# Optimization experiments

Measured on AMD Instinct MI355X. Metric: run time of the kernel, lower is better.

Reference implementation:

```python
import jax, jax.numpy as jnp
import numpy as np

NPOINT, NSAMPLE, RADIUS = 2048, 32, 0.2
EPS = 1e-5


def setup_inputs() -> dict:
    key = jax.random.key(0)
    ks = jax.random.split(key, 12)
    B, N, C = 8, 8192, 64
    mlp = [64, 64, 128]
    inp = {
        "xyz": jax.random.normal(ks[0], (B, 3, N), dtype=jnp.float32),
        "points": jax.random.normal(ks[1], (B, C, N), dtype=jnp.float32),
    }
    last = C + 3  # use_xyz concatenates 3 relative coords
    for i, out in enumerate(mlp, 1):
        inp[f"W{i}"] = jax.random.normal(ks[2 * i], (out, last), dtype=jnp.float32) / np.sqrt(last).astype(np.float32)
        inp[f"b{i}"] = jnp.zeros((out,), jnp.float32)
        inp[f"g{i}"] = jnp.ones((out,), jnp.float32)
        inp[f"be{i}"] = jnp.zeros((out,), jnp.float32)
        last = out
    return inp


def fps(xyz_t, npoint):
    """Farthest point sampling. xyz_t: (B,N,3) -> (B,npoint) int32 indices."""
    xyz_t = jax.lax.stop_gradient(xyz_t)  # indices are non-differentiable
    B, N, _ = xyz_t.shape

    def step(carry, _):
        dists, far = carry  # (B,N), (B,)
        cent = jnp.take_along_axis(xyz_t, far[:, None, None], axis=1)  # (B,1,3)
        d = jnp.sum((xyz_t - cent) ** 2, axis=-1)
        dists = jnp.minimum(dists, d)
        nf = jnp.argmax(dists, axis=-1).astype(jnp.int32)
        return (dists, nf), far

    init = (jnp.full((B, N), 1e10, xyz_t.dtype), jnp.zeros((B,), jnp.int32))
    _, idxs = jax.lax.scan(step, init, None, length=npoint)
    return jnp.transpose(idxs)  # (B, npoint)


def ball_query(xyz_t, new_xyz_t, radius, nsample):
    """First-nsample-in-radius neighbor indices, padded with first hit.
    xyz_t (B,N,3), new_xyz_t (B,M,3) -> (B,M,nsample) int32."""
    B, N, _ = xyz_t.shape
    # squared distances via gemm to avoid (B,M,N,3) intermediate
    sq = (jnp.sum(new_xyz_t ** 2, -1)[:, :, None]
          + jnp.sum(xyz_t ** 2, -1)[:, None, :]
          - 2.0 * jnp.einsum('bmd,bnd->bmn', new_xyz_t, xyz_t))  # (B,M,N)
    cand = jnp.where(sq < radius * radius, jnp.arange(N, dtype=jnp.int32), N)
    idx = jnp.sort(cand, axis=-1)[:, :, :nsample]  # first k in-radius by index order
    first = idx[:, :, :1]
    first = jnp.where(first == N, 0, first)  # guard empty groups
    idx = jnp.where(idx == N, first, idx)
    return idx


def group(feat, idx):
    """feat (B,C,N), idx (B,M,k) -> (B,C,M,k) gathered neighbor features."""
    return jnp.take_along_axis(feat[:, :, None, :], idx[:, None, :, :], axis=3)


def conv_bn_relu(x, W, b, g, be):
    """Shared 1x1 Conv2d + BatchNorm2d (batch stats, training mode) + ReLU.
    x: (B,C,M,K) -> (B,O,M,K)."""
    y = jnp.einsum('oc,bcmk->bomk', W, x) + b[None, :, None, None]
    mu = jnp.mean(y, axis=(0, 2, 3), keepdims=True)
    var = jnp.var(y, axis=(0, 2, 3), keepdims=True)
    y = (y - mu) * jax.lax.rsqrt(var + EPS)
    y = y * g[None, :, None, None] + be[None, :, None, None]
    return jax.nn.relu(y)


def reference(xyz, points, W1, b1, g1, be1, W2, b2, g2, be2, W3, b3, g3, be3):
    xyz_t = jnp.transpose(xyz, (0, 2, 1))  # (B,N,3)
    fidx = fps(xyz_t, NPOINT)  # (B,M)
    new_xyz = jnp.take_along_axis(xyz, fidx[:, None, :], axis=2)  # (B,3,M)
    idx = ball_query(xyz_t, jnp.transpose(new_xyz, (0, 2, 1)), RADIUS, NSAMPLE)  # (B,M,K)
    grouped_xyz = group(xyz, idx) - new_xyz[:, :, :, None]  # (B,3,M,K) centered
    grouped_pts = group(points, idx)  # (B,f,M,K)
    x = jnp.concatenate([grouped_xyz, grouped_pts], axis=1)  # (B,f+3,M,K)
    x = conv_bn_relu(x, W1, b1, g1, be1)
    x = conv_bn_relu(x, W2, b2, g2, be2)
    x = conv_bn_relu(x, W3, b3, g3, be3)
    new_points = jnp.max(x, axis=3)  # (B,mlp[-1],M)
    return (new_xyz, new_points)
```

## Files before the change

### kernel.cpp

```cpp
#include <hip/hip_runtime.h>

#define BB 8
#define NN 8192
#define MM 2048
#define KK 32
#define NTOT (BB*MM*KK)

#define WS_PTS_T  0
#define WS_XYZN   4194304
#define WS_IDX    5242880
#define WS_GPART  5767168
#define WS_PARAMS 6291456
#define WS_ZMAX   6292480
#define WS_ZMIN   8389632
#define WS_TOTAL  10486784

typedef float v2f __attribute__((ext_vector_type(2)));

__global__ __launch_bounds__(256) void k_transpose(const float* __restrict__ pts,
                                                   float* __restrict__ pts_t){
  __shared__ float tile[64][65];
  int bid = blockIdx.x;
  int b = bid >> 7;
  int n0 = (bid & 127) << 6;
  int tx = threadIdx.x & 63, ty = threadIdx.x >> 6;
  const float* src = pts + (size_t)b*64*NN;
  #pragma unroll
  for (int c = ty; c < 64; c += 4)
    tile[c][tx] = src[(size_t)c*NN + n0 + tx];
  __syncthreads();
  float* dst = pts_t + ((size_t)b*NN + n0)*64;
  #pragma unroll
  for (int r = ty; r < 64; r += 4)
    dst[(size_t)r*64 + tx] = tile[tx][r];
}

__global__ __launch_bounds__(256) void k_xyzn(const float* __restrict__ xyz,
                                              float4* __restrict__ xyzn){
  #pragma clang fp contract(off)
  int i = blockIdx.x*256 + threadIdx.x;
  int b = i >> 13, n = i & 8191;
  const float* p = xyz + (size_t)b*3*NN;
  float x = p[n], y = p[NN+n], z = p[2*NN+n];
  float nrm = (x*x + y*y) + z*z;
  xyzn[i] = make_float4(x, y, z, nrm);
}

#define DPPMAXF(ctrl, rmask)                                                 \
  {                                                                          \
    float s_ = __int_as_float(__builtin_amdgcn_update_dpp(                   \
        __float_as_int(m), __float_as_int(m), (ctrl), (rmask), 0xf, false)); \
    m = fmaxf(m, s_);                                                        \
  }

__global__ __launch_bounds__(256,1) void k_fps(const float* __restrict__ xyz,
                                               float* __restrict__ out_newxyz){
  #pragma clang fp contract(off)
  __shared__ float4 sp4[NN];
  __shared__ unsigned long long swk[2][4];
  int b = blockIdx.x, tid = threadIdx.x;
  const float* xb = xyz + (size_t)b*3*NN;
  int n0 = tid << 5;
  v2f px[16], py[16], pz[16], dd[16];
  const float4* xb4 = (const float4*)xb;
  #pragma unroll
  for (int q = 0; q < 8; ++q){
    float4 X = xb4[(n0>>2) + q];
    float4 Y = xb4[(NN>>2) + (n0>>2) + q];
    float4 Z = xb4[((2*NN)>>2) + (n0>>2) + q];
    px[2*q]   = (v2f){X.x, X.y}; px[2*q+1] = (v2f){X.z, X.w};
    py[2*q]   = (v2f){Y.x, Y.y}; py[2*q+1] = (v2f){Y.z, Y.w};
    pz[2*q]   = (v2f){Z.x, Z.y}; pz[2*q+1] = (v2f){Z.z, Z.w};
    dd[2*q]   = (v2f){1e10f,1e10f}; dd[2*q+1] = (v2f){1e10f,1e10f};
    sp4[n0+4*q+0] = make_float4(X.x, Y.x, Z.x, 0.f);
    sp4[n0+4*q+1] = make_float4(X.y, Y.y, Z.y, 0.f);
    sp4[n0+4*q+2] = make_float4(X.z, Y.z, Z.z, 0.f);
    sp4[n0+4*q+3] = make_float4(X.w, Y.w, Z.w, 0.f);
  }
  __syncthreads();
  float4 c0 = sp4[0];
  float cx = c0.x, cy = c0.y, cz = c0.z;
  float* ob = out_newxyz + (size_t)b*3*MM;
  int lane = tid & 63, wid = tid >> 6;
  for (int s = 0; s < 8; ++s){
    float ox = 0.f, oy = 0.f, oz = 0.f;
    #pragma unroll 1
    for (int ti = 0; ti < 256; ++ti){
      if (tid == ti){ ox = cx; oy = cy; oz = cz; }
      v2f cvx = (v2f){cx,cx}, cvy = (v2f){cy,cy}, cvz = (v2f){cz,cz};
      v2f bv2 = (v2f){-1.f,-1.f};
      #pragma unroll
      for (int g = 0; g < 16; ++g){
        v2f dx = px[g]-cvx, dy = py[g]-cvy, dz = pz[g]-cvz;
        v2f xx = dx*dx, yy = dy*dy, zz = dz*dz;
        v2f sm = xx + yy;
        v2f d  = sm + zz;
        v2f nd = __builtin_elementwise_min(dd[g], d);
        dd[g] = nd;
        bv2 = __builtin_elementwise_max(bv2, nd);
      }
      float bv = fmaxf(bv2.x, bv2.y);
      float m = bv;
      DPPMAXF(0x111, 0xf)
      DPPMAXF(0x112, 0xf)
      DPPMAXF(0x114, 0xf)
      DPPMAXF(0x118, 0xf)
      DPPMAXF(0x142, 0xa)
      DPPMAXF(0x143, 0xc)
      float wm = __int_as_float(__builtin_amdgcn_readlane(__float_as_int(m), 63));
      unsigned long long msk = __ballot(bv == wm);
      int wl = (int)__builtin_ctzll(msk);
      int bj = 0;
      #pragma unroll
      for (int g = 15; g >= 0; --g){
        if (dd[g].y == bv) bj = 2*g+1;
        if (dd[g].x == bv) bj = 2*g;
      }
      int nwin = __builtin_amdgcn_readlane(n0 + bj, wl);
      int buf = ti & 1;
      if (lane == 0){
        unsigned long long key =
            ((unsigned long long)__float_as_uint(wm) << 32) |
            (unsigned int)(~(unsigned int)nwin);
        swk[buf][wid] = key;
      }
      __syncthreads();
      const unsigned long long* kk = swk[buf];
      unsigned long long k0=kk[0], k1=kk[1], k2=kk[2], k3=kk[3];
      unsigned long long a = (k0>k1)?k0:k1, c2 = (k2>k3)?k2:k3;
      unsigned long long kmax = (a>c2)?a:c2;
      int far = (int)(~(unsigned int)kmax) & (NN-1);
      float4 c4 = sp4[far];
      cx = c4.x; cy = c4.y; cz = c4.z;
    }
    ob[(s<<8)+tid] = ox; ob[MM+(s<<8)+tid] = oy; ob[2*MM+(s<<8)+tid] = oz;
  }
}

__global__ __launch_bounds__(256) void k_ballq(const float4* __restrict__ xyzn,
                                               const float* __restrict__ newxyz,
                                               int* __restrict__ idx){
  #pragma clang fp contract(off)
  __shared__ unsigned long long s_mask[32][129];
  __shared__ float4 s_c4[32];
  const float R2 = (float)(0.2*0.2);
  int b = blockIdx.x >> 6;
  int m0 = (blockIdx.x & 63) << 5;
  int tid = threadIdx.x, lane = tid & 63, wv = tid >> 6;
  const float* nb = newxyz + (size_t)b*3*MM;
  if (tid < 32){
    int m = m0 + tid;
    float cx = nb[m], cy = nb[MM+m], cz = nb[2*MM+m];
    float cn = (cx*cx + cy*cy) + cz*cz;
    s_c4[tid] = make_float4(cx, cy, cz, cn);
  }
  __syncthreads();
  const float4* src = xyzn + (size_t)b*NN;
  for (int ci = 0; ci < 32; ++ci){
    int ch = ci*4 + wv;
    float4 p = src[ch*64 + lane];
    #pragma unroll 8
    for (int mi = 0; mi < 32; ++mi){
      float4 c = s_c4[mi];
      float dot = (c.x*p.x + c.y*p.y) + c.z*p.z;
      float sq = (c.w + p.w) - 2.0f*dot;
      unsigned long long mk = __ballot(sq < R2);
      if (lane == 0) s_mask[mi][ch] = mk;
    }
  }
  __syncthreads();
  if (tid < 32){
    int m = m0 + tid;
    int* om = idx + ((size_t)(b*MM + m))*KK;
    int filled = 0, first = -1;
    for (int ch = 0; ch < 128 && filled < KK; ++ch){
      unsigned long long mk = s_mask[tid][ch];
      while (mk){
        int bp = __builtin_ctzll(mk);
        mk &= mk - 1;
        int j = ch*64 + bp;
        if (first < 0) first = j;
        om[filled++] = j;
        if (filled == KK) break;
      }
    }
    int pad = (first < 0) ? 0 : first;
    for (int s = filled; s < KK; ++s) om[s] = pad;
  }
}

#define XST 260
#define PST 66

__device__ __forceinline__ void fma_po(float4& a0, float4& a1, float w,
                                       const float4& xA, const float4& xB){
  a0.x = fmaf(w, xA.x, a0.x); a0.y = fmaf(w, xA.y, a0.y);
  a0.z = fmaf(w, xA.z, a0.z); a0.w = fmaf(w, xA.w, a0.w);
  a1.x = fmaf(w, xB.x, a1.x); a1.y = fmaf(w, xB.y, a1.y);
  a1.z = fmaf(w, xB.z, a1.z); a1.w = fmaf(w, xB.w, a1.w);
}

__device__ __forceinline__ void gemm_step(float4 (&acc)[8][2], const float* sw,
                                          const float* sx, int c, int ob8, int pb){
  float4 xA = *(const float4*)&sx[c*XST + pb];
  float4 xB = *(const float4*)&sx[c*XST + pb + 4];
  float4 wA = *(const float4*)&sw[c*64 + ob8];
  float4 wB = *(const float4*)&sw[c*64 + ob8 + 4];
  fma_po(acc[0][0], acc[0][1], wA.x, xA, xB);
  fma_po(acc[1][0], acc[1][1], wA.y, xA, xB);
  fma_po(acc[2][0], acc[2][1], wA.z, xA, xB);
  fma_po(acc[3][0], acc[3][1], wA.w, xA, xB);
  fma_po(acc[4][0], acc[4][1], wB.x, xA, xB);
  fma_po(acc[5][0], acc[5][1], wB.y, xA, xB);
  fma_po(acc[6][0], acc[6][1], wB.z, xA, xB);
  fma_po(acc[7][0], acc[7][1], wB.w, xA, xB);
}

__device__ __forceinline__ void gather_col(float* sx, const float* pts_t,
    const float4* xyzn, const float* nb, const int* idx, int b, int bid, int tid){
  int m0 = (bid & 255) << 3;
  int m = m0 + (tid >> 5), k = tid & 31;
  int j = idx[((size_t)(b*MM + m))*KK + k];
  float4 P = xyzn[(size_t)b*NN + j];
  sx[0*XST + tid] = P.x - nb[m];
  sx[1*XST + tid] = P.y - nb[MM+m];
  sx[2*XST + tid] = P.z - nb[2*MM+m];
  const float4* pf = (const float4*)(pts_t + ((size_t)b*NN + j)*64);
  #pragma unroll
  for (int c4 = 0; c4 < 16; ++c4){
    float4 v = pf[c4];
    sx[(3+4*c4+0)*XST + tid] = v.x;
    sx[(3+4*c4+1)*XST + tid] = v.y;
    sx[(3+4*c4+2)*XST + tid] = v.z;
    sx[(3+4*c4+3)*XST + tid] = v.w;
  }
}

__device__ __forceinline__ void tile_stats(const float4 (&acc)[8][2], float* s_pp,
    float* gpart, int ob8, int pg, int tid, int bid, int nch_base){
  #pragma unroll
  for (int oi = 0; oi < 8; ++oi){
    float4 a0 = acc[oi][0], a1 = acc[oi][1];
    float s  = ((a0.x+a0.y)+(a0.z+a0.w)) + ((a1.x+a1.y)+(a1.z+a1.w));
    float q2 = ((a0.x*a0.x + a0.y*a0.y) + (a0.z*a0.z + a0.w*a0.w))
             + ((a1.x*a1.x + a1.y*a1.y) + (a1.z*a1.z + a1.w*a1.w));
    int o = ob8 + oi;
    s_pp[o*PST + pg*2 + 0] = s;
    s_pp[o*PST + pg*2 + 1] = q2;
  }
  __syncthreads();
  if (tid < 128){
    int o = tid >> 1, st = tid & 1;
    float S = 0.f;
    #pragma unroll 8
    for (int q = 0; q < 32; ++q) S += s_pp[o*PST + q*2 + st];
    gpart[(size_t)(st*128 + nch_base + o)*2048 + bid] = S;
  }
}

__global__ __launch_bounds__(256,1) void k_conv1_stats(const float* __restrict__ pts_t,
    const float4* __restrict__ xyzn, const float* __restrict__ newxyz,
    const int* __restrict__ idx, const float* __restrict__ W1, float* __restrict__ gpart){
  __shared__ float s_w1[67*64];
  __shared__ float s_x[67*XST];
  int tid = threadIdx.x;
  for (int i = tid; i < 67*64; i += 256){ int c = i>>6, o = i&63; s_w1[i] = W1[o*67 + c]; }
  int bid = blockIdx.x, b = bid >> 8;
  const float* nb = newxyz + (size_t)b*3*MM;
  gather_col(s_x, pts_t, xyzn, nb, idx, b, bid, tid);
  __syncthreads();
  int oq = tid & 7, pg = tid >> 3;
  int ob8 = oq*8, pb = pg*8;
  float4 acc[8][2];
  #pragma unroll
  for (int oi=0;oi<8;++oi){ acc[oi][0]=make_float4(0,0,0,0); acc[oi][1]=make_float4(0,0,0,0); }
  for (int c = 0; c < 67; ++c) gemm_step(acc, s_w1, s_x, c, ob8, pb);
  __syncthreads();
  tile_stats(acc, s_x, gpart, ob8, pg, tid, bid, 0);
}

__global__ __launch_bounds__(256,1) void k_conv2_stats(const float* __restrict__ pts_t,
    const float4* __restrict__ xyzn, const float* __restrict__ newxyz,
    const int* __restrict__ idx, const float* __restrict__ W1, const float* __restrict__ W2,
    const float* __restrict__ params1, float* __restrict__ gpart){
  __shared__ float s_w1[67*64];
  __shared__ float s_w2[64*64];
  __shared__ float s_p[128];
  __shared__ float s_x[67*XST];
  int tid = threadIdx.x;
  for (int i = tid; i < 67*64; i += 256){ int c = i>>6, o = i&63; s_w1[i] = W1[o*67 + c]; }
  for (int i = tid; i < 64*64; i += 256){ int c = i>>6, o = i&63; s_w2[i] = W2[o*64 + c]; }
  if (tid < 64){ s_p[tid] = params1[tid]; s_p[64+tid] = params1[128+tid]; }
  int bid = blockIdx.x, b = bid >> 8;
  const float* nb = newxyz + (size_t)b*3*MM;
  gather_col(s_x, pts_t, xyzn, nb, idx, b, bid, tid);
  __syncthreads();
  int oq = tid & 7, pg = tid >> 3;
  int ob8 = oq*8, pb = pg*8;
  float4 acc[8][2];
  #pragma unroll
  for (int oi=0;oi<8;++oi){ acc[oi][0]=make_float4(0,0,0,0); acc[oi][1]=make_float4(0,0,0,0); }
  for (int c = 0; c < 67; ++c) gemm_step(acc, s_w1, s_x, c, ob8, pb);
  float4 hreg[8][2];
  #pragma unroll
  for (int oi = 0; oi < 8; ++oi){
    float A = s_p[ob8+oi], C = s_p[64+ob8+oi];
    float4 z0 = acc[oi][0], z1 = acc[oi][1], h0, h1;
    h0.x = fmaxf(fmaf(A, z0.x, C), 0.f); h0.y = fmaxf(fmaf(A, z0.y, C), 0.f);
    h0.z = fmaxf(fmaf(A, z0.z, C), 0.f); h0.w = fmaxf(fmaf(A, z0.w, C), 0.f);
    h1.x = fmaxf(fmaf(A, z1.x, C), 0.f); h1.y = fmaxf(fmaf(A, z1.y, C), 0.f);
    h1.z = fmaxf(fmaf(A, z1.z, C), 0.f); h1.w = fmaxf(fmaf(A, z1.w, C), 0.f);
    hreg[oi][0] = h0; hreg[oi][1] = h1;
  }
  __syncthreads();
  #pragma unroll
  for (int oi = 0; oi < 8; ++oi){
    *(float4*)&s_x[(ob8+oi)*XST + pb]     = hreg[oi][0];
    *(float4*)&s_x[(ob8+oi)*XST + pb + 4] = hreg[oi][1];
  }
  __syncthreads();
  #pragma unroll
  for (int oi=0;oi<8;++oi){ acc[oi][0]=make_float4(0,0,0,0); acc[oi][1]=make_float4(0,0,0,0); }
  for (int c = 0; c < 64; ++c) gemm_step(acc, s_w2, s_x, c, ob8, pb);
  __syncthreads();
  tile_stats(acc, s_x, gpart, ob8, pg, tid, bid, 0);
}

__device__ __forceinline__ void accum_ch(float4* acc, const float4* w4, int c, float v){
  #pragma unroll
  for (int o4 = 0; o4 < 16; ++o4){
    float4 w = w4[c*16 + o4];
    acc[o4].x = fmaf(w.x, v, acc[o4].x);
    acc[o4].y = fmaf(w.y, v, acc[o4].y);
    acc[o4].z = fmaf(w.z, v, acc[o4].z);
    acc[o4].w = fmaf(w.w, v, acc[o4].w);
  }
}

__device__ __forceinline__ void conv1_pos(float4* acc, const float* s_w1,
    const float* pts_t, const float4* xyzn, const float* nb, int b, int m, int j){
  #pragma unroll
  for (int o4 = 0; o4 < 16; ++o4) acc[o4] = make_float4(0.f,0.f,0.f,0.f);
  float4 P = xyzn[(size_t)b*NN + j];
  float x0 = P.x - nb[m], x1 = P.y - nb[MM+m], x2 = P.z - nb[2*MM+m];
  const float4* w4 = (const float4*)s_w1;
  accum_ch(acc, w4, 0, x0);
  accum_ch(acc, w4, 1, x1);
  accum_ch(acc, w4, 2, x2);
  const float4* pf = (const float4*)(pts_t + ((size_t)b*NN + j)*64);
  #pragma unroll
  for (int c4 = 0; c4 < 16; ++c4){
    float4 v = pf[c4];
    accum_ch(acc, w4, 3+4*c4+0, v.x);
    accum_ch(acc, w4, 3+4*c4+1, v.y);
    accum_ch(acc, w4, 3+4*c4+2, v.z);
    accum_ch(acc, w4, 3+4*c4+3, v.w);
  }
}

__global__ __launch_bounds__(256) void k_bnfin(const float* __restrict__ gpart,
    const float* __restrict__ g, const float* __restrict__ be, float* __restrict__ params){
  int o = blockIdx.x, t = threadIdx.x;
  double s = 0.0, sq = 0.0;
  for (int i = t; i < 2048; i += 256){
    s  += (double)gpart[(size_t)o*2048 + i];
    sq += (double)gpart[(size_t)(128+o)*2048 + i];
  }
  __shared__ double ds[256], dq[256];
  ds[t] = s; dq[t] = sq; __syncthreads();
  for (int off = 128; off > 0; off >>= 1){
    if (t < off){ ds[t] += ds[t+off]; dq[t] += dq[t+off]; }
    __syncthreads();
  }
  if (t == 0){
    double mu = ds[0] / (double)NTOT;
    double var = dq[0] / (double)NTOT - mu*mu;
    float A = g[o] / sqrtf((float)var + 1e-5f);
    float Cc = be[o] - (float)mu * A;
    params[o] = A; params[128+o] = Cc;
  }
}

__global__ __launch_bounds__(256,1) void k_conv3(const float* __restrict__ pts_t,
    const float4* __restrict__ xyzn, const float* __restrict__ newxyz,
    const int* __restrict__ idx, const float* __restrict__ W1, const float* __restrict__ W2,
    const float* __restrict__ W3, const float* __restrict__ params1,
    const float* __restrict__ params2, float* __restrict__ gpart,
    float* __restrict__ zmax, float* __restrict__ zmin){
  __shared__ float s_w1[67*64];
  __shared__ float s_w2[64*64];
  __shared__ float s_p[256];
  __shared__ float s_z[256*68];
  __shared__ float s_sm[8*128*2];
  int tid = threadIdx.x;
  for (int i = tid; i < 67*64; i += 256){ int c = i>>6, o = i&63; s_w1[i] = W1[o*67 + c]; }
  for (int i = tid; i < 64*64; i += 256){ int c = i>>6, o = i&63; s_w2[i] = W2[o*64 + c]; }
  if (tid < 64){
    s_p[tid]      = params1[tid];     s_p[64+tid]  = params1[128+tid];
    s_p[128+tid]  = params2[tid];     s_p[192+tid] = params2[128+tid];
  }
  __syncthreads();
  int bid = blockIdx.x, b = bid >> 8, m0 = (bid & 255) << 3;
  {
    int m = m0 + (tid >> 5), k = tid & 31;
    int j = idx[((size_t)(b*MM + m))*KK + k];
    const float* nb = newxyz + (size_t)b*3*MM;
    float4 acc[16];
    conv1_pos(acc, s_w1, pts_t, xyzn, nb, b, m, j);
    float4 h[16];
    #pragma unroll
    for (int o4 = 0; o4 < 16; ++o4){
      float4 z = acc[o4], hh;
      hh.x = fmaxf(fmaf(s_p[4*o4+0], z.x, s_p[64+4*o4+0]), 0.f);
      hh.y = fmaxf(fmaf(s_p[4*o4+1], z.y, s_p[64+4*o4+1]), 0.f);
      hh.z = fmaxf(fmaf(s_p[4*o4+2], z.z, s_p[64+4*o4+2]), 0.f);
      hh.w = fmaxf(fmaf(s_p[4*o4+3], z.w, s_p[64+4*o4+3]), 0.f);
      h[o4] = hh;
    }
    float4 a2[16];
    #pragma unroll
    for (int o4 = 0; o4 < 16; ++o4) a2[o4] = make_float4(0.f,0.f,0.f,0.f);
    const float4* w24 = (const float4*)s_w2;
    #pragma unroll
    for (int c4 = 0; c4 < 16; ++c4){
      accum_ch(a2, w24, 4*c4+0, h[c4].x);
      accum_ch(a2, w24, 4*c4+1, h[c4].y);
      accum_ch(a2, w24, 4*c4+2, h[c4].z);
      accum_ch(a2, w24, 4*c4+3, h[c4].w);
    }
    #pragma unroll
    for (int o4 = 0; o4 < 16; ++o4){
      float4 z = a2[o4], hh;
      hh.x = fmaxf(fmaf(s_p[128+4*o4+0], z.x, s_p[192+4*o4+0]), 0.f);
      hh.y = fmaxf(fmaf(s_p[128+4*o4+1], z.y, s_p[192+4*o4+1]), 0.f);
      hh.z = fmaxf(fmaf(s_p[128+4*o4+2], z.z, s_p[192+4*o4+2]), 0.f);
      hh.w = fmaxf(fmaf(s_p[128+4*o4+3], z.w, s_p[192+4*o4+3]), 0.f);
      *(float4*)&s_z[tid*68 + o4*4] = hh;
    }
  }
  __syncthreads();
  int ml = tid >> 5, og = tid & 31;
  float accK[4][32];
  #pragma unroll
  for (int oo = 0; oo < 4; ++oo)
    #pragma unroll
    for (int k2 = 0; k2 < 32; ++k2) accK[oo][k2] = 0.f;
  const float4* w3g = (const float4*)W3;
  #pragma unroll
  for (int c4 = 0; c4 < 16; ++c4){
    float4 w[4];
    #pragma unroll
    for (int oo = 0; oo < 4; ++oo) w[oo] = w3g[(og*4+oo)*16 + c4];
    #pragma unroll
    for (int k2 = 0; k2 < 32; ++k2){
      float4 hv = *(const float4*)&s_z[(ml*32+k2)*68 + c4*4];
      #pragma unroll
      for (int oo = 0; oo < 4; ++oo){
        accK[oo][k2] = fmaf(w[oo].x, hv.x, accK[oo][k2]);
        accK[oo][k2] = fmaf(w[oo].y, hv.y, accK[oo][k2]);
        accK[oo][k2] = fmaf(w[oo].z, hv.z, accK[oo][k2]);
        accK[oo][k2] = fmaf(w[oo].w, hv.w, accK[oo][k2]);
      }
    }
  }
  int m = m0 + ml;
  #pragma unroll
  for (int oo = 0; oo < 4; ++oo){
    float mx = -3.4e38f, mn = 3.4e38f, s = 0.f, sq = 0.f;
    #pragma unroll
    for (int k2 = 0; k2 < 32; ++k2){
      float v = accK[oo][k2];
      mx = fmaxf(mx, v); mn = fminf(mn, v);
      s += v; sq = fmaf(v, v, sq);
    }
    int o = og*4 + oo;
    zmax[((size_t)(b*128 + o))*MM + m] = mx;
    zmin[((size_t)(b*128 + o))*MM + m] = mn;
    s_sm[(ml*128+o)*2] = s; s_sm[(ml*128+o)*2+1] = sq;
  }
  __syncthreads();
  {
    int o = tid >> 1, st = tid & 1;
    float S = 0.f;
    #pragma unroll
    for (int mm = 0; mm < 8; ++mm) S += s_sm[(mm*128+o)*2 + st];
    gpart[(size_t)(st*128+o)*2048 + bid] = S;
  }
}

__global__ __launch_bounds__(256) void k_out(const float* __restrict__ zmax,
    const float* __restrict__ zmin, const float* __restrict__ params3,
    float* __restrict__ out){
  int i = blockIdx.x*256 + threadIdx.x;
  int o = (i >> 11) & 127;
  float A = params3[o], Cc = params3[128+o];
  float v = (A >= 0.f) ? fmaf(A, zmax[i], Cc) : fmaf(A, zmin[i], Cc);
  out[49152 + i] = fmaxf(v, 0.f);
}

extern "C" void kernel_launch(void* const* d_in, const int* in_sizes, int n_in,
                              void* d_out, int out_size, void* d_ws, size_t ws_size,
                              hipStream_t stream){
  const float* xyz    = (const float*)d_in[0];
  const float* points = (const float*)d_in[1];
  const float* W1  = (const float*)d_in[2];
  const float* g1  = (const float*)d_in[4];
  const float* be1 = (const float*)d_in[5];
  const float* W2  = (const float*)d_in[6];
  const float* g2  = (const float*)d_in[8];
  const float* be2 = (const float*)d_in[9];
  const float* W3  = (const float*)d_in[10];
  const float* g3  = (const float*)d_in[12];
  const float* be3 = (const float*)d_in[13];

  if (ws_size < (size_t)WS_TOTAL * sizeof(float)) return;

  float*  ws     = (float*)d_ws;
  float*  pts_t  = ws + WS_PTS_T;
  float4* xyzn   = (float4*)(ws + WS_XYZN);
  int*    idx    = (int*)(ws + WS_IDX);
  float*  gpart  = ws + WS_GPART;
  float*  params = ws + WS_PARAMS;
  float*  zmax   = ws + WS_ZMAX;
  float*  zmin   = ws + WS_ZMIN;
  float*  out    = (float*)d_out;
  float*  newxyz = out;

  hipLaunchKernelGGL(k_fps,       dim3(8),    dim3(256), 0, stream, xyz, newxyz);
  hipLaunchKernelGGL(k_transpose, dim3(1024), dim3(256), 0, stream, points, pts_t);
  hipLaunchKernelGGL(k_xyzn,      dim3(256),  dim3(256), 0, stream, xyz, xyzn);
  hipLaunchKernelGGL(k_ballq,     dim3(512),  dim3(256), 0, stream, xyzn, newxyz, idx);
  hipLaunchKernelGGL(k_conv1_stats, dim3(2048), dim3(256), 0, stream,
                     pts_t, xyzn, newxyz, idx, W1, gpart);
  hipLaunchKernelGGL(k_bnfin, dim3(64), dim3(256), 0, stream, gpart, g1, be1, params+0);
  hipLaunchKernelGGL(k_conv2_stats, dim3(2048), dim3(256), 0, stream,
                     pts_t, xyzn, newxyz, idx, W1, W2, params+0, gpart);
  hipLaunchKernelGGL(k_bnfin, dim3(64), dim3(256), 0, stream, gpart, g2, be2, params+256);
  hipLaunchKernelGGL(k_conv3, dim3(2048), dim3(256), 0, stream,
                     pts_t, xyzn, newxyz, idx, W1, W2, W3, params+0, params+256,
                     gpart, zmax, zmin);
  hipLaunchKernelGGL(k_bnfin, dim3(128), dim3(256), 0, stream, gpart, g3, be3, params+512);
  hipLaunchKernelGGL(k_out, dim3(8192), dim3(256), 0, stream, zmax, zmin, params+512, out);
}
```

Baseline: 2.792 ms.

## Process two batches per FPS block with 512 threads; tile conv3 GEMMs via shared memory

FPS now runs 4 blocks of 512 threads, each handling two batch items with interleaved updates and reductions. Each thread holds 16 points instead of 32, and centroid coordinates are read from the global xyzn buffer instead of an LDS copy, so k_xyzn now launches before FPS. This targets FPS's serial per-iteration latency by overlapping two independent dependency chains, at the cost of more registers and 8-wave reductions. Separately, conv3 replaces its per-thread 67→64→64 recompute with the shared-memory tiled gather/GEMM path used by conv2, and stages W3 in LDS, which raises LDS use per block.

```diff
diff --git a/kernel.cpp b/kernel.cpp
--- a/kernel.cpp
+++ b/kernel.cpp
@@ -46,94 +46,120 @@
   xyzn[i] = make_float4(x, y, z, nrm);
 }
 
-#define DPPMAXF(ctrl, rmask)                                                 \
-  {                                                                          \
-    float s_ = __int_as_float(__builtin_amdgcn_update_dpp(                   \
-        __float_as_int(m), __float_as_int(m), (ctrl), (rmask), 0xf, false)); \
-    m = fmaxf(m, s_);                                                        \
-  }
-
-__global__ __launch_bounds__(256,1) void k_fps(const float* __restrict__ xyz,
+__device__ __forceinline__ float wave_max_f32(float v){
+#define WMSTEP(c,r) { float s_ = __int_as_float(__builtin_amdgcn_update_dpp(   \
+      __float_as_int(v), __float_as_int(v), (c), (r), 0xf, false));            \
+    v = fmaxf(v, s_); }
+  WMSTEP(0x111, 0xf)
+  WMSTEP(0x112, 0xf)
+  WMSTEP(0x114, 0xf)
+  WMSTEP(0x118, 0xf)
+  WMSTEP(0x142, 0xa)
+  WMSTEP(0x143, 0xc)
+#undef WMSTEP
+  return __int_as_float(__builtin_amdgcn_readlane(__float_as_int(v), 63));
+}
+
+__device__ __forceinline__ float fps_update(v2f* px, v2f* py, v2f* pz, v2f* dd,
+                                            float cx, float cy, float cz){
+  v2f cvx = (v2f){cx,cx}, cvy = (v2f){cy,cy}, cvz = (v2f){cz,cz};
+  v2f bv2 = (v2f){-1.f,-1.f};
+  #pragma unroll
+  for (int g = 0; g < 8; ++g){
+    v2f dx = px[g]-cvx, dy = py[g]-cvy, dz = pz[g]-cvz;
+    v2f xx = dx*dx, yy = dy*dy, zz = dz*dz;
+    v2f sm = xx + yy;
+    v2f d  = sm + zz;
+    v2f nd = __builtin_elementwise_min(dd[g], d);
+    dd[g] = nd;
+    bv2 = __builtin_elementwise_max(bv2, nd);
+  }
+  return fmaxf(bv2.x, bv2.y);
+}
+
+__device__ __forceinline__ void fps_reduce(float bv, const v2f* dd, int n0,
+    int lane, int wid, unsigned long long* swk){
+  float wm = wave_max_f32(bv);
+  unsigned long long msk = __ballot(bv == wm);
+  int wl = (int)__builtin_ctzll(msk);
+  int bj = 0;
+  #pragma unroll
+  for (int g = 7; g >= 0; --g){
+    if (dd[g].y == bv) bj = 2*g+1;
+    if (dd[g].x == bv) bj = 2*g;
+  }
+  int nw = __builtin_amdgcn_readlane(n0 + bj, wl);
+  if (lane == 0)
+    swk[wid] = ((unsigned long long)__float_as_uint(wm) << 32) |
+               (unsigned int)(~(unsigned int)nw);
+}
+
+__device__ __forceinline__ unsigned long long tree8(const unsigned long long* k){
+  unsigned long long a = (k[0]>k[1])?k[0]:k[1], b = (k[2]>k[3])?k[2]:k[3];
+  unsigned long long c = (k[4]>k[5])?k[4]:k[5], d = (k[6]>k[7])?k[6]:k[7];
+  unsigned long long e = (a>b)?a:b, f = (c>d)?c:d;
+  return (e>f)?e:f;
+}
+
+__global__ __launch_bounds__(512,1) void k_fps(const float* __restrict__ xyz,
+                                               const float4* __restrict__ xyzn,
                                                float* __restrict__ out_newxyz){
   #pragma clang fp contract(off)
-  __shared__ float4 sp4[NN];
-  __shared__ unsigned long long swk[2][4];
-  int b = blockIdx.x, tid = threadIdx.x;
-  const float* xb = xyz + (size_t)b*3*NN;
-  int n0 = tid << 5;
-  v2f px[16], py[16], pz[16], dd[16];
+  __shared__ unsigned long long swk[2][2][8];
+  int tid = threadIdx.x, lane = tid & 63, wid = tid >> 6;
+  int bA = blockIdx.x*2, bB = bA + 1;
+  const float* xa = xyz + (size_t)bA*3*NN;
+  const float* xb = xyz + (size_t)bB*3*NN;
+  int n0 = tid << 4;
+  v2f pxA[8],pyA[8],pzA[8],ddA[8];
+  v2f pxB[8],pyB[8],pzB[8],ddB[8];
+  const float4* xa4 = (const float4*)xa;
   const float4* xb4 = (const float4*)xb;
   #pragma unroll
-  for (int q = 0; q < 8; ++q){
-    float4 X = xb4[(n0>>2) + q];
-    float4 Y = xb4[(NN>>2) + (n0>>2) + q];
-    float4 Z = xb4[((2*NN)>>2) + (n0>>2) + q];
-    px[2*q]   = (v2f){X.x, X.y}; px[2*q+1] = (v2f){X.z, X.w};
-    py[2*q]   = (v2f){Y.x, Y.y}; py[2*q+1] = (v2f){Y.z, Y.w};
-    pz[2*q]   = (v2f){Z.x, Z.y}; pz[2*q+1] = (v2f){Z.z, Z.w};
-    dd[2*q]   = (v2f){1e10f,1e10f}; dd[2*q+1] = (v2f){1e10f,1e10f};
-    sp4[n0+4*q+0] = make_float4(X.x, Y.x, Z.x, 0.f);
-    sp4[n0+4*q+1] = make_float4(X.y, Y.y, Z.y, 0.f);
-    sp4[n0+4*q+2] = make_float4(X.z, Y.z, Z.z, 0.f);
-    sp4[n0+4*q+3] = make_float4(X.w, Y.w, Z.w, 0.f);
-  }
-  __syncthreads();
-  float4 c0 = sp4[0];
-  float cx = c0.x, cy = c0.y, cz = c0.z;
-  float* ob = out_newxyz + (size_t)b*3*MM;
-  int lane = tid & 63, wid = tid >> 6;
-  for (int s = 0; s < 8; ++s){
-    float ox = 0.f, oy = 0.f, oz = 0.f;
+  for (int q = 0; q < 4; ++q){
+    float4 X = xa4[(n0>>2)+q];
+    float4 Y = xa4[(NN>>2)+(n0>>2)+q];
+    float4 Z = xa4[((2*NN)>>2)+(n0>>2)+q];
+    pxA[2*q] = (v2f){X.x,X.y}; pxA[2*q+1] = (v2f){X.z,X.w};
+    pyA[2*q] = (v2f){Y.x,Y.y}; pyA[2*q+1] = (v2f){Y.z,Y.w};
+    pzA[2*q] = (v2f){Z.x,Z.y}; pzA[2*q+1] = (v2f){Z.z,Z.w};
+    ddA[2*q] = (v2f){1e10f,1e10f}; ddA[2*q+1] = (v2f){1e10f,1e10f};
+    X = xb4[(n0>>2)+q];
+    Y = xb4[(NN>>2)+(n0>>2)+q];
+    Z = xb4[((2*NN)>>2)+(n0>>2)+q];
+    pxB[2*q] = (v2f){X.x,X.y}; pxB[2*q+1] = (v2f){X.z,X.w};
+    pyB[2*q] = (v2f){Y.x,Y.y}; pyB[2*q+1] = (v2f){Y.z,Y.w};
+    pzB[2*q] = (v2f){Z.x,Z.y}; pzB[2*q+1] = (v2f){Z.z,Z.w};
+    ddB[2*q] = (v2f){1e10f,1e10f}; ddB[2*q+1] = (v2f){1e10f,1e10f};
+  }
+  float4 c0A = xyzn[(size_t)bA*NN];
+  float4 c0B = xyzn[(size_t)bB*NN];
+  float cxA=c0A.x, cyA=c0A.y, czA=c0A.z;
+  float cxB=c0B.x, cyB=c0B.y, czB=c0B.z;
+  float* obA = out_newxyz + (size_t)bA*3*MM;
+  float* obB = out_newxyz + (size_t)bB*3*MM;
+  for (int s = 0; s < 4; ++s){
+    float oxA=0,oyA=0,ozA=0, oxB=0,oyB=0,ozB=0;
     #pragma unroll 1
-    for (int ti = 0; ti < 256; ++ti){
-      if (tid == ti){ ox = cx; oy = cy; oz = cz; }
-      v2f cvx = (v2f){cx,cx}, cvy = (v2f){cy,cy}, cvz = (v2f){cz,cz};
-      v2f bv2 = (v2f){-1.f,-1.f};
-      #pragma unroll
-      for (int g = 0; g < 16; ++g){
-        v2f dx = px[g]-cvx, dy = py[g]-cvy, dz = pz[g]-cvz;
-        v2f xx = dx*dx, yy = dy*dy, zz = dz*dz;
-        v2f sm = xx + yy;
-        v2f d  = sm + zz;
-        v2f nd = __builtin_elementwise_min(dd[g], d);
-        dd[g] = nd;
-        bv2 = __builtin_elementwise_max(bv2, nd);
-      }
-      float bv = fmaxf(bv2.x, bv2.y);
-      float m = bv;
-      DPPMAXF(0x111, 0xf)
-      DPPMAXF(0x112, 0xf)
-      DPPMAXF(0x114, 0xf)
-      DPPMAXF(0x118, 0xf)
-      DPPMAXF(0x142, 0xa)
-      DPPMAXF(0x143, 0xc)
-      float wm = __int_as_float(__builtin_amdgcn_readlane(__float_as_int(m), 63));
-      unsigned long long msk = __ballot(bv == wm);
-      int wl = (int)__builtin_ctzll(msk);
-      int bj = 0;
-      #pragma unroll
-      for (int g = 15; g >= 0; --g){
-        if (dd[g].y == bv) bj = 2*g+1;
-        if (dd[g].x == bv) bj = 2*g;
-      }
-      int nwin = __builtin_amdgcn_readlane(n0 + bj, wl);
+    for (int ti = 0; ti < 512; ++ti){
+      if (tid == ti){ oxA=cxA; oyA=cyA; ozA=czA; oxB=cxB; oyB=cyB; ozB=czB; }
+      float bvA = fps_update(pxA,pyA,pzA,ddA, cxA,cyA,czA);
+      float bvB = fps_update(pxB,pyB,pzB,ddB, cxB,cyB,czB);
       int buf = ti & 1;
-      if (lane == 0){
-        unsigned long long key =
-            ((unsigned long long)__float_as_uint(wm) << 32) |
-            (unsigned int)(~(unsigned int)nwin);
-        swk[buf][wid] = key;
-      }
+      fps_reduce(bvA, ddA, n0, lane, wid, swk[buf][0]);
+      fps_reduce(bvB, ddB, n0, lane, wid, swk[buf][1]);
       __syncthreads();
-      const unsigned long long* kk = swk[buf];
-      unsigned long long k0=kk[0], k1=kk[1], k2=kk[2], k3=kk[3];
-      unsigned long long a = (k0>k1)?k0:k1, c2 = (k2>k3)?k2:k3;
-      unsigned long long kmax = (a>c2)?a:c2;
-      int far = (int)(~(unsigned int)kmax) & (NN-1);
-      float4 c4 = sp4[far];
-      cx = c4.x; cy = c4.y; cz = c4.z;
+      unsigned long long kmA = tree8(swk[buf][0]);
+      unsigned long long kmB = tree8(swk[buf][1]);
+      int farA = (int)(~(unsigned int)kmA) & (NN-1);
+      int farB = (int)(~(unsigned int)kmB) & (NN-1);
+      float4 c4A = xyzn[(size_t)bA*NN + farA];
+      float4 c4B = xyzn[(size_t)bB*NN + farB];
+      cxA=c4A.x; cyA=c4A.y; czA=c4A.z;
+      cxB=c4B.x; cyB=c4B.y; czB=c4B.z;
     }
-    ob[(s<<8)+tid] = ox; ob[MM+(s<<8)+tid] = oy; ob[2*MM+(s<<8)+tid] = oz;
+    obA[(s<<9)+tid] = oxA; obA[MM+(s<<9)+tid] = oyA; obA[2*MM+(s<<9)+tid] = ozA;
+    obB[(s<<9)+tid] = oxB; obB[MM+(s<<9)+tid] = oyB; obB[2*MM+(s<<9)+tid] = ozB;
   }
 }
 
@@ -236,6 +262,29 @@
   }
 }
 
+__device__ __forceinline__ void bnrelu_tile(float4 (&acc)[8][2], const float* sA,
+                                            const float* sC, int ob8){
+  #pragma unroll
+  for (int oi = 0; oi < 8; ++oi){
+    float A = sA[ob8+oi], C = sC[ob8+oi];
+    float4 z0 = acc[oi][0], z1 = acc[oi][1];
+    z0.x = fmaxf(fmaf(A, z0.x, C), 0.f); z0.y = fmaxf(fmaf(A, z0.y, C), 0.f);
+    z0.z = fmaxf(fmaf(A, z0.z, C), 0.f); z0.w = fmaxf(fmaf(A, z0.w, C), 0.f);
+    z1.x = fmaxf(fmaf(A, z1.x, C), 0.f); z1.y = fmaxf(fmaf(A, z1.y, C), 0.f);
+    z1.z = fmaxf(fmaf(A, z1.z, C), 0.f); z1.w = fmaxf(fmaf(A, z1.w, C), 0.f);
+    acc[oi][0] = z0; acc[oi][1] = z1;
+  }
+}
+
+__device__ __forceinline__ void stash_tile(const float4 (&acc)[8][2], float* sx,
+                                           int ob8, int pb){
+  #pragma unroll
+  for (int oi = 0; oi < 8; ++oi){
+    *(float4*)&sx[(ob8+oi)*XST + pb]     = acc[oi][0];
+    *(float4*)&sx[(ob8+oi)*XST + pb + 4] = acc[oi][1];
+  }
+}
+
 __device__ __forceinline__ void tile_stats(const float4 (&acc)[8][2], float* s_pp,
     float* gpart, int ob8, int pg, int tid, int bid, int nch_base){
   #pragma unroll
@@ -301,61 +350,15 @@
   #pragma unroll
   for (int oi=0;oi<8;++oi){ acc[oi][0]=make_float4(0,0,0,0); acc[oi][1]=make_float4(0,0,0,0); }
   for (int c = 0; c < 67; ++c) gemm_step(acc, s_w1, s_x, c, ob8, pb);
-  float4 hreg[8][2];
-  #pragma unroll
-  for (int oi = 0; oi < 8; ++oi){
-    float A = s_p[ob8+oi], C = s_p[64+ob8+oi];
-    float4 z0 = acc[oi][0], z1 = acc[oi][1], h0, h1;
-    h0.x = fmaxf(fmaf(A, z0.x, C), 0.f); h0.y = fmaxf(fmaf(A, z0.y, C), 0.f);
-    h0.z = fmaxf(fmaf(A, z0.z, C), 0.f); h0.w = fmaxf(fmaf(A, z0.w, C), 0.f);
-    h1.x = fmaxf(fmaf(A, z1.x, C), 0.f); h1.y = fmaxf(fmaf(A, z1.y, C), 0.f);
-    h1.z = fmaxf(fmaf(A, z1.z, C), 0.f); h1.w = fmaxf(fmaf(A, z1.w, C), 0.f);
-    hreg[oi][0] = h0; hreg[oi][1] = h1;
-  }
-  __syncthreads();
-  #pragma unroll
-  for (int oi = 0; oi < 8; ++oi){
-    *(float4*)&s_x[(ob8+oi)*XST + pb]     = hreg[oi][0];
-    *(float4*)&s_x[(ob8+oi)*XST + pb + 4] = hreg[oi][1];
-  }
+  bnrelu_tile(acc, s_p, s_p+64, ob8);
+  __syncthreads();
+  stash_tile(acc, s_x, ob8, pb);
   __syncthreads();
   #pragma unroll
   for (int oi=0;oi<8;++oi){ acc[oi][0]=make_float4(0,0,0,0); acc[oi][1]=make_float4(0,0,0,0); }
   for (int c = 0; c < 64; ++c) gemm_step(acc, s_w2, s_x, c, ob8, pb);
   __syncthreads();
   tile_stats(acc, s_x, gpart, ob8, pg, tid, bid, 0);
-}
-
-__device__ __forceinline__ void accum_ch(float4* acc, const float4* w4, int c, float v){
-  #pragma unroll
-  for (int o4 = 0; o4 < 16; ++o4){
-    float4 w = w4[c*16 + o4];
-    acc[o4].x = fmaf(w.x, v, acc[o4].x);
-    acc[o4].y = fmaf(w.y, v, acc[o4].y);
-    acc[o4].z = fmaf(w.z, v, acc[o4].z);
-    acc[o4].w = fmaf(w.w, v, acc[o4].w);
-  }
-}
-
-__device__ __forceinline__ void conv1_pos(float4* acc, const float* s_w1,
-    const float* pts_t, const float4* xyzn, const float* nb, int b, int m, int j){
-  #pragma unroll
-  for (int o4 = 0; o4 < 16; ++o4) acc[o4] = make_float4(0.f,0.f,0.f,0.f);
-  float4 P = xyzn[(size_t)b*NN + j];
-  float x0 = P.x - nb[m], x1 = P.y - nb[MM+m], x2 = P.z - nb[2*MM+m];
-  const float4* w4 = (const float4*)s_w1;
-  accum_ch(acc, w4, 0, x0);
-  accum_ch(acc, w4, 1, x1);
-  accum_ch(acc, w4, 2, x2);
-  const float4* pf = (const float4*)(pts_t + ((size_t)b*NN + j)*64);
-  #pragma unroll
-  for (int c4 = 0; c4 < 16; ++c4){
-    float4 v = pf[c4];
-    accum_ch(acc, w4, 3+4*c4+0, v.x);
-    accum_ch(acc, w4, 3+4*c4+1, v.y);
-    accum_ch(acc, w4, 3+4*c4+2, v.z);
-    accum_ch(acc, w4, 3+4*c4+3, v.w);
-  }
 }
 
 __global__ __launch_bounds__(256) void k_bnfin(const float* __restrict__ gpart,
@@ -389,55 +392,38 @@
     float* __restrict__ zmax, float* __restrict__ zmin){
   __shared__ float s_w1[67*64];
   __shared__ float s_w2[64*64];
+  __shared__ float s_w3[64*128];
   __shared__ float s_p[256];
-  __shared__ float s_z[256*68];
+  __shared__ float s_x[67*XST];
   __shared__ float s_sm[8*128*2];
   int tid = threadIdx.x;
   for (int i = tid; i < 67*64; i += 256){ int c = i>>6, o = i&63; s_w1[i] = W1[o*67 + c]; }
   for (int i = tid; i < 64*64; i += 256){ int c = i>>6, o = i&63; s_w2[i] = W2[o*64 + c]; }
+  for (int i = tid; i < 64*128; i += 256){ int c = i>>7, o = i&127; s_w3[c*128+o] = W3[o*64 + c]; }
   if (tid < 64){
     s_p[tid]      = params1[tid];     s_p[64+tid]  = params1[128+tid];
     s_p[128+tid]  = params2[tid];     s_p[192+tid] = params2[128+tid];
   }
-  __syncthreads();
   int bid = blockIdx.x, b = bid >> 8, m0 = (bid & 255) << 3;
-  {
-    int m = m0 + (tid >> 5), k = tid & 31;
-    int j = idx[((size_t)(b*MM + m))*KK + k];
-    const float* nb = newxyz + (size_t)b*3*MM;
-    float4 acc[16];
-    conv1_pos(acc, s_w1, pts_t, xyzn, nb, b, m, j);
-    float4 h[16];
-    #pragma unroll
-    for (int o4 = 0; o4 < 16; ++o4){
-      float4 z = acc[o4], hh;
-      hh.x = fmaxf(fmaf(s_p[4*o4+0], z.x, s_p[64+4*o4+0]), 0.f);
-      hh.y = fmaxf(fmaf(s_p[4*o4+1], z.y, s_p[64+4*o4+1]), 0.f);
-      hh.z = fmaxf(fmaf(s_p[4*o4+2], z.z, s_p[64+4*o4+2]), 0.f);
-      hh.w = fmaxf(fmaf(s_p[4*o4+3], z.w, s_p[64+4*o4+3]), 0.f);
-      h[o4] = hh;
-    }
-    float4 a2[16];
-    #pragma unroll
-    for (int o4 = 0; o4 < 16; ++o4) a2[o4] = make_float4(0.f,0.f,0.f,0.f);
-    const float4* w24 = (const float4*)s_w2;
-    #pragma unroll
-    for (int c4 = 0; c4 < 16; ++c4){
-      accum_ch(a2, w24, 4*c4+0, h[c4].x);
-      accum_ch(a2, w24, 4*c4+1, h[c4].y);
-      accum_ch(a2, w24, 4*c4+2, h[c4].z);
-      accum_ch(a2, w24, 4*c4+3, h[c4].w);
-    }
-    #pragma unroll
-    for (int o4 = 0; o4 < 16; ++o4){
-      float4 z = a2[o4], hh;
-      hh.x = fmaxf(fmaf(s_p[128+4*o4+0], z.x, s_p[192+4*o4+0]), 0.f);
-      hh.y = fmaxf(fmaf(s_p[128+4*o4+1], z.y, s_p[192+4*o4+1]), 0.f);
-      hh.z = fmaxf(fmaf(s_p[128+4*o4+2], z.z, s_p[192+4*o4+2]), 0.f);
-      hh.w = fmaxf(fmaf(s_p[128+4*o4+3], z.w, s_p[192+4*o4+3]), 0.f);
-      *(float4*)&s_z[tid*68 + o4*4] = hh;
-    }
-  }
+  const float* nb = newxyz + (size_t)b*3*MM;
+  gather_col(s_x, pts_t, xyzn, nb, idx, b, bid, tid);
+  __syncthreads();
+  int oq = tid & 7, pg = tid >> 3;
+  int ob8 = oq*8, pb = pg*8;
+  float4 acc[8][2];
+  #pragma unroll
+  for (int oi=0;oi<8;++oi){ acc[oi][0]=make_float4(0,0,0,0); acc[oi][1]=make_float4(0,0,0,0); }
+  for (int c = 0; c < 67; ++c) gemm_step(acc, s_w1, s_x, c, ob8, pb);
+  bnrelu_tile(acc, s_p, s_p+64, ob8);
+  __syncthreads();
+  stash_tile(acc, s_x, ob8, pb);
+  __syncthreads();
+  #pragma unroll
+  for (int oi=0;oi<8;++oi){ acc[oi][0]=make_float4(0,0,0,0); acc[oi][1]=make_float4(0,0,0,0); }
+  for (int c = 0; c < 64; ++c) gemm_step(acc, s_w2, s_x, c, ob8, pb);
+  bnrelu_tile(acc, s_p+128, s_p+192, ob8);
+  __syncthreads();
+  stash_tile(acc, s_x, ob8, pb);
   __syncthreads();
   int ml = tid >> 5, og = tid & 31;
   float accK[4][32];
@@ -445,21 +431,19 @@
   for (int oo = 0; oo < 4; ++oo)
     #pragma unroll
     for (int k2 = 0; k2 < 32; ++k2) accK[oo][k2] = 0.f;
-  const float4* w3g = (const float4*)W3;
-  #pragma unroll
-  for (int c4 = 0; c4 < 16; ++c4){
-    float4 w[4];
+  for (int c = 0; c < 64; ++c){
+    float4 w = *(const float4*)&s_w3[c*128 + og*4];
     #pragma unroll
-    for (int oo = 0; oo < 4; ++oo) w[oo] = w3g[(og*4+oo)*16 + c4];
-    #pragma unroll
-    for (int k2 = 0; k2 < 32; ++k2){
-      float4 hv = *(const float4*)&s_z[(ml*32+k2)*68 + c4*4];
+    for (int q = 0; q < 8; ++q){
+      float4 xv = *(const float4*)&s_x[c*XST + ml*32 + q*4];
+      float xs4[4] = {xv.x, xv.y, xv.z, xv.w};
       #pragma unroll
-      for (int oo = 0; oo < 4; ++oo){
-        accK[oo][k2] = fmaf(w[oo].x, hv.x, accK[oo][k2]);
-        accK[oo][k2] = fmaf(w[oo].y, hv.y, accK[oo][k2]);
-        accK[oo][k2] = fmaf(w[oo].z, hv.z, accK[oo][k2]);
-        accK[oo][k2] = fmaf(w[oo].w, hv.w, accK[oo][k2]);
+      for (int j = 0; j < 4; ++j){
+        float xs = xs4[j];
+        accK[0][q*4+j] = fmaf(w.x, xs, accK[0][q*4+j]);
+        accK[1][q*4+j] = fmaf(w.y, xs, accK[1][q*4+j]);
+        accK[2][q*4+j] = fmaf(w.z, xs, accK[2][q*4+j]);
+        accK[3][q*4+j] = fmaf(w.w, xs, accK[3][q*4+j]);
       }
     }
   }
@@ -526,9 +510,9 @@
   float*  out    = (float*)d_out;
   float*  newxyz = out;
 
-  hipLaunchKernelGGL(k_fps,       dim3(8),    dim3(256), 0, stream, xyz, newxyz);
+  hipLaunchKernelGGL(k_xyzn,      dim3(256),  dim3(256), 0, stream, xyz, xyzn);
   hipLaunchKernelGGL(k_transpose, dim3(1024), dim3(256), 0, stream, points, pts_t);
-  hipLaunchKernelGGL(k_xyzn,      dim3(256),  dim3(256), 0, stream, xyz, xyzn);
+  hipLaunchKernelGGL(k_fps,       dim3(4),    dim3(512), 0, stream, xyz, xyzn, newxyz);
   hipLaunchKernelGGL(k_ballq,     dim3(512),  dim3(256), 0, stream, xyzn, newxyz, idx);
   hipLaunchKernelGGL(k_conv1_stats, dim3(2048), dim3(256), 0, stream,
                      pts_t, xyzn, newxyz, idx, W1, gpart);
```

Measured after the change: 4.445 ms. 1.59x slower.

## Restructure conv3 kernel to use shared-memory tiled GEMMs for conv1/conv2

Applied to the files above, without the earlier changes.

The fused conv3 kernel previously had each thread compute all 64 channels for one point from global gathers, and read W3 from global memory. It now gathers the point columns into shared memory and runs the 8x8 register-tiled GEMM path used by the stats kernel for conv1 and conv2, staging the activations in shared memory. W3 is also copied into shared memory in channel-major layout for the third layer. This aims to cut per-thread register pressure and redundant shared/global weight loads, at the cost of more shared memory (reducing occupancy) and extra barriers.

```diff
diff --git a/kernel.cpp b/kernel.cpp
--- a/kernel.cpp
+++ b/kernel.cpp
@@ -236,6 +236,29 @@
   }
 }
 
+__device__ __forceinline__ void bnrelu_tile(float4 (&acc)[8][2], const float* sA,
+                                            const float* sC, int ob8){
+  #pragma unroll
+  for (int oi = 0; oi < 8; ++oi){
+    float A = sA[ob8+oi], C = sC[ob8+oi];
+    float4 z0 = acc[oi][0], z1 = acc[oi][1];
+    z0.x = fmaxf(fmaf(A, z0.x, C), 0.f); z0.y = fmaxf(fmaf(A, z0.y, C), 0.f);
+    z0.z = fmaxf(fmaf(A, z0.z, C), 0.f); z0.w = fmaxf(fmaf(A, z0.w, C), 0.f);
+    z1.x = fmaxf(fmaf(A, z1.x, C), 0.f); z1.y = fmaxf(fmaf(A, z1.y, C), 0.f);
+    z1.z = fmaxf(fmaf(A, z1.z, C), 0.f); z1.w = fmaxf(fmaf(A, z1.w, C), 0.f);
+    acc[oi][0] = z0; acc[oi][1] = z1;
+  }
+}
+
+__device__ __forceinline__ void stash_tile(const float4 (&acc)[8][2], float* sx,
+                                           int ob8, int pb){
+  #pragma unroll
+  for (int oi = 0; oi < 8; ++oi){
+    *(float4*)&sx[(ob8+oi)*XST + pb]     = acc[oi][0];
+    *(float4*)&sx[(ob8+oi)*XST + pb + 4] = acc[oi][1];
+  }
+}
+
 __device__ __forceinline__ void tile_stats(const float4 (&acc)[8][2], float* s_pp,
     float* gpart, int ob8, int pg, int tid, int bid, int nch_base){
   #pragma unroll
@@ -301,61 +324,15 @@
   #pragma unroll
   for (int oi=0;oi<8;++oi){ acc[oi][0]=make_float4(0,0,0,0); acc[oi][1]=make_float4(0,0,0,0); }
   for (int c = 0; c < 67; ++c) gemm_step(acc, s_w1, s_x, c, ob8, pb);
-  float4 hreg[8][2];
-  #pragma unroll
-  for (int oi = 0; oi < 8; ++oi){
-    float A = s_p[ob8+oi], C = s_p[64+ob8+oi];
-    float4 z0 = acc[oi][0], z1 = acc[oi][1], h0, h1;
-    h0.x = fmaxf(fmaf(A, z0.x, C), 0.f); h0.y = fmaxf(fmaf(A, z0.y, C), 0.f);
-    h0.z = fmaxf(fmaf(A, z0.z, C), 0.f); h0.w = fmaxf(fmaf(A, z0.w, C), 0.f);
-    h1.x = fmaxf(fmaf(A, z1.x, C), 0.f); h1.y = fmaxf(fmaf(A, z1.y, C), 0.f);
-    h1.z = fmaxf(fmaf(A, z1.z, C), 0.f); h1.w = fmaxf(fmaf(A, z1.w, C), 0.f);
-    hreg[oi][0] = h0; hreg[oi][1] = h1;
-  }
-  __syncthreads();
-  #pragma unroll
-  for (int oi = 0; oi < 8; ++oi){
-    *(float4*)&s_x[(ob8+oi)*XST + pb]     = hreg[oi][0];
-    *(float4*)&s_x[(ob8+oi)*XST + pb + 4] = hreg[oi][1];
-  }
+  bnrelu_tile(acc, s_p, s_p+64, ob8);
+  __syncthreads();
+  stash_tile(acc, s_x, ob8, pb);
   __syncthreads();
   #pragma unroll
   for (int oi=0;oi<8;++oi){ acc[oi][0]=make_float4(0,0,0,0); acc[oi][1]=make_float4(0,0,0,0); }
   for (int c = 0; c < 64; ++c) gemm_step(acc, s_w2, s_x, c, ob8, pb);
   __syncthreads();
   tile_stats(acc, s_x, gpart, ob8, pg, tid, bid, 0);
-}
-
-__device__ __forceinline__ void accum_ch(float4* acc, const float4* w4, int c, float v){
-  #pragma unroll
-  for (int o4 = 0; o4 < 16; ++o4){
-    float4 w = w4[c*16 + o4];
-    acc[o4].x = fmaf(w.x, v, acc[o4].x);
-    acc[o4].y = fmaf(w.y, v, acc[o4].y);
-    acc[o4].z = fmaf(w.z, v, acc[o4].z);
-    acc[o4].w = fmaf(w.w, v, acc[o4].w);
-  }
-}
-
-__device__ __forceinline__ void conv1_pos(float4* acc, const float* s_w1,
-    const float* pts_t, const float4* xyzn, const float* nb, int b, int m, int j){
-  #pragma unroll
-  for (int o4 = 0; o4 < 16; ++o4) acc[o4] = make_float4(0.f,0.f,0.f,0.f);
-  float4 P = xyzn[(size_t)b*NN + j];
-  float x0 = P.x - nb[m], x1 = P.y - nb[MM+m], x2 = P.z - nb[2*MM+m];
-  const float4* w4 = (const float4*)s_w1;
-  accum_ch(acc, w4, 0, x0);
-  accum_ch(acc, w4, 1, x1);
-  accum_ch(acc, w4, 2, x2);
-  const float4* pf = (const float4*)(pts_t + ((size_t)b*NN + j)*64);
-  #pragma unroll
-  for (int c4 = 0; c4 < 16; ++c4){
-    float4 v = pf[c4];
-    accum_ch(acc, w4, 3+4*c4+0, v.x);
-    accum_ch(acc, w4, 3+4*c4+1, v.y);
-    accum_ch(acc, w4, 3+4*c4+2, v.z);
-    accum_ch(acc, w4, 3+4*c4+3, v.w);
-  }
 }
 
 __global__ __launch_bounds__(256) void k_bnfin(const float* __restrict__ gpart,
@@ -389,55 +366,38 @@
     float* __restrict__ zmax, float* __restrict__ zmin){
   __shared__ float s_w1[67*64];
   __shared__ float s_w2[64*64];
+  __shared__ float s_w3[64*128];
   __shared__ float s_p[256];
-  __shared__ float s_z[256*68];
+  __shared__ float s_x[67*XST];
   __shared__ float s_sm[8*128*2];
   int tid = threadIdx.x;
   for (int i = tid; i < 67*64; i += 256){ int c = i>>6, o = i&63; s_w1[i] = W1[o*67 + c]; }
   for (int i = tid; i < 64*64; i += 256){ int c = i>>6, o = i&63; s_w2[i] = W2[o*64 + c]; }
+  for (int i = tid; i < 64*128; i += 256){ int c = i>>7, o = i&127; s_w3[c*128+o] = W3[o*64 + c]; }
   if (tid < 64){
     s_p[tid]      = params1[tid];     s_p[64+tid]  = params1[128+tid];
     s_p[128+tid]  = params2[tid];     s_p[192+tid] = params2[128+tid];
   }
-  __syncthreads();
   int bid = blockIdx.x, b = bid >> 8, m0 = (bid & 255) << 3;
-  {
-    int m = m0 + (tid >> 5), k = tid & 31;
-    int j = idx[((size_t)(b*MM + m))*KK + k];
-    const float* nb = newxyz + (size_t)b*3*MM;
-    float4 acc[16];
-    conv1_pos(acc, s_w1, pts_t, xyzn, nb, b, m, j);
-    float4 h[16];
-    #pragma unroll
-    for (int o4 = 0; o4 < 16; ++o4){
-      float4 z = acc[o4], hh;
-      hh.x = fmaxf(fmaf(s_p[4*o4+0], z.x, s_p[64+4*o4+0]), 0.f);
-      hh.y = fmaxf(fmaf(s_p[4*o4+1], z.y, s_p[64+4*o4+1]), 0.f);
-      hh.z = fmaxf(fmaf(s_p[4*o4+2], z.z, s_p[64+4*o4+2]), 0.f);
-      hh.w = fmaxf(fmaf(s_p[4*o4+3], z.w, s_p[64+4*o4+3]), 0.f);
-      h[o4] = hh;
-    }
-    float4 a2[16];
-    #pragma unroll
-    for (int o4 = 0; o4 < 16; ++o4) a2[o4] = make_float4(0.f,0.f,0.f,0.f);
-    const float4* w24 = (const float4*)s_w2;
-    #pragma unroll
-    for (int c4 = 0; c4 < 16; ++c4){
-      accum_ch(a2, w24, 4*c4+0, h[c4].x);
-      accum_ch(a2, w24, 4*c4+1, h[c4].y);
-      accum_ch(a2, w24, 4*c4+2, h[c4].z);
-      accum_ch(a2, w24, 4*c4+3, h[c4].w);
-    }
-    #pragma unroll
-    for (int o4 = 0; o4 < 16; ++o4){
-      float4 z = a2[o4], hh;
-      hh.x = fmaxf(fmaf(s_p[128+4*o4+0], z.x, s_p[192+4*o4+0]), 0.f);
-      hh.y = fmaxf(fmaf(s_p[128+4*o4+1], z.y, s_p[192+4*o4+1]), 0.f);
-      hh.z = fmaxf(fmaf(s_p[128+4*o4+2], z.z, s_p[192+4*o4+2]), 0.f);
-      hh.w = fmaxf(fmaf(s_p[128+4*o4+3], z.w, s_p[192+4*o4+3]), 0.f);
-      *(float4*)&s_z[tid*68 + o4*4] = hh;
-    }
-  }
+  const float* nb = newxyz + (size_t)b*3*MM;
+  gather_col(s_x, pts_t, xyzn, nb, idx, b, bid, tid);
+  __syncthreads();
+  int oq = tid & 7, pg = tid >> 3;
+  int ob8 = oq*8, pb = pg*8;
+  float4 acc[8][2];
+  #pragma unroll
+  for (int oi=0;oi<8;++oi){ acc[oi][0]=make_float4(0,0,0,0); acc[oi][1]=make_float4(0,0,0,0); }
+  for (int c = 0; c < 67; ++c) gemm_step(acc, s_w1, s_x, c, ob8, pb);
+  bnrelu_tile(acc, s_p, s_p+64, ob8);
+  __syncthreads();
+  stash_tile(acc, s_x, ob8, pb);
+  __syncthreads();
+  #pragma unroll
+  for (int oi=0;oi<8;++oi){ acc[oi][0]=make_float4(0,0,0,0); acc[oi][1]=make_float4(0,0,0,0); }
+  for (int c = 0; c < 64; ++c) gemm_step(acc, s_w2, s_x, c, ob8, pb);
+  bnrelu_tile(acc, s_p+128, s_p+192, ob8);
+  __syncthreads();
+  stash_tile(acc, s_x, ob8, pb);
   __syncthreads();
   int ml = tid >> 5, og = tid & 31;
   float accK[4][32];
@@ -445,21 +405,19 @@
   for (int oo = 0; oo < 4; ++oo)
     #pragma unroll
     for (int k2 = 0; k2 < 32; ++k2) accK[oo][k2] = 0.f;
-  const float4* w3g = (const float4*)W3;
-  #pragma unroll
-  for (int c4 = 0; c4 < 16; ++c4){
-    float4 w[4];
+  for (int c = 0; c < 64; ++c){
+    float4 w = *(const float4*)&s_w3[c*128 + og*4];
     #pragma unroll
-    for (int oo = 0; oo < 4; ++oo) w[oo] = w3g[(og*4+oo)*16 + c4];
-    #pragma unroll
-    for (int k2 = 0; k2 < 32; ++k2){
-      float4 hv = *(const float4*)&s_z[(ml*32+k2)*68 + c4*4];
+    for (int q = 0; q < 8; ++q){
+      float4 xv = *(const float4*)&s_x[c*XST + ml*32 + q*4];
+      float xs4[4] = {xv.x, xv.y, xv.z, xv.w};
       #pragma unroll
-      for (int oo = 0; oo < 4; ++oo){
-        accK[oo][k2] = fmaf(w[oo].x, hv.x, accK[oo][k2]);
-        accK[oo][k2] = fmaf(w[oo].y, hv.y, accK[oo][k2]);
-        accK[oo][k2] = fmaf(w[oo].z, hv.z, accK[oo][k2]);
-        accK[oo][k2] = fmaf(w[oo].w, hv.w, accK[oo][k2]);
+      for (int j = 0; j < 4; ++j){
+        float xs = xs4[j];
+        accK[0][q*4+j] = fmaf(w.x, xs, accK[0][q*4+j]);
+        accK[1][q*4+j] = fmaf(w.y, xs, accK[1][q*4+j]);
+        accK[2][q*4+j] = fmaf(w.z, xs, accK[2][q*4+j]);
+        accK[3][q*4+j] = fmaf(w.w, xs, accK[3][q*4+j]);
       }
     }
   }
```

Result: faster. 2.604 ms (-6.7%).
